# Kernel optimization log

Measured on AMD Instinct MI355X. Metric: run time of the kernel, lower is better.

The kernel has to match this reference:

```python
import jax, jax.numpy as jnp
import numpy as np

N_NODES = 100000


def setup_inputs() -> dict:
    key = jax.random.key(0)
    k1, k2, k3, k4 = jax.random.split(key, 4)
    N, E, D_IN, D_OUT = N_NODES, 3200000, 256, 256
    feature = jax.random.normal(k1, (N, D_IN), dtype=jnp.float32)
    edge_src = jax.random.randint(k2, (E,), 0, N, dtype=jnp.int32)
    edge_dst = jax.random.randint(k3, (E,), 0, N, dtype=jnp.int32)
    W = jax.random.normal(k4, (D_IN, D_OUT), dtype=jnp.float32) * (1.0 / np.sqrt(D_IN))
    b = jnp.zeros((D_OUT,), dtype=jnp.float32)
    return {"feature": feature, "edge_src": edge_src, "edge_dst": edge_dst, "W": W, "b": b}


def reference(feature, edge_src, edge_dst, W, b):
    # update_all(copy_src('h','m'), sum('m','h')): for each node i,
    # h_i = sum over edges (j->i) of feature[j]  -- scatter-add by destination.
    msgs = feature[edge_src]                                   # [E, D_in] (gather)
    agg = jax.ops.segment_sum(msgs, edge_dst, num_segments=N_NODES)  # [N, D_in]
    # apply_nodes: Linear + activation (relu)
    h = jnp.dot(agg, W) + b                                    # [N, D_out]
    return jax.nn.relu(h)
```

## Files before the change

### kernel.cpp

```cpp
#include <hip/hip_runtime.h>

#define D 256
#define GSHIFT 4
#define GSIZE 16
#define TN 16
#define CAPG2 1024
#define CSHIFT 8
#define CBIN 256
#define GPB 16
#define NCMAX 512
#define CAPC 9216
#define NB_P 256

using bf16x8 = __attribute__((ext_vector_type(8))) short;
using f32x4  = __attribute__((ext_vector_type(4))) float;

__device__ inline float bf_lo(unsigned int u) {
    return __builtin_bit_cast(float, u << 16);
}
__device__ inline float bf_hi(unsigned int u) {
    return __builtin_bit_cast(float, u & 0xffff0000u);
}
__device__ inline unsigned short f2bf(float f) {
    unsigned int x = __builtin_bit_cast(unsigned int, f);
    unsigned int r = (x + 0x7fffu + ((x >> 16) & 1u)) >> 16;
    return (unsigned short)r;
}

__global__ __launch_bounds__(256) void part_kernel(
    const int* __restrict__ src, const int* __restrict__ dst,
    int* __restrict__ gcntC, int* __restrict__ csrA,
    const float* __restrict__ feature, unsigned short* __restrict__ fbf, long n8,
    const float* __restrict__ W, unsigned short* __restrict__ Wt,
    int E, int NC, int chunk, int nConvF)
{
    __shared__ int h[NCMAX];
    const int b = blockIdx.x, t = threadIdx.x;

    if (b < NB_P) {
        for (int i = t; i < NC; i += 256) h[i] = 0;
        __syncthreads();
        const int beg = b * chunk;
        const int end = min(beg + chunk, E);
        for (int i = beg + t; i < end; i += 256)
            atomicAdd(&h[dst[i] >> CSHIFT], 1);
        __syncthreads();
        for (int i = t; i < NC; i += 256) {
            int c = h[i];
            h[i] = c ? atomicAdd(&gcntC[i], c) : 0;
        }
        __syncthreads();
        for (int i = beg + t; i < end; i += 256) {
            int d = dst[i];
            int c = d >> CSHIFT;
            int r = atomicAdd(&h[c], 1);
            if (r < CAPC)
                csrA[(size_t)c * CAPC + r] = (src[i] << CSHIFT) | (d & (CBIN - 1));
        }
        return;
    }
    if (b < NB_P + nConvF) {
        long i = (long)(b - NB_P) * 256 + t;
        if (i < n8) {
            const float4* p = reinterpret_cast<const float4*>(feature + i * 8);
            float4 v0 = p[0], v1 = p[1];
            uint4 r;
            r.x = (unsigned int)f2bf(v0.x) | ((unsigned int)f2bf(v0.y) << 16);
            r.y = (unsigned int)f2bf(v0.z) | ((unsigned int)f2bf(v0.w) << 16);
            r.z = (unsigned int)f2bf(v1.x) | ((unsigned int)f2bf(v1.y) << 16);
            r.w = (unsigned int)f2bf(v1.z) | ((unsigned int)f2bf(v1.w) << 16);
            *reinterpret_cast<uint4*>(fbf + i * 8) = r;
        }
        return;
    }
    int i = (b - NB_P - nConvF) * 256 + t;
    if (i < D * D / 4) {
        int n  = i >> 6;
        int k0 = (i & 63) * 4;
        float a  = W[(size_t)(k0 + 0) * D + n];
        float bb = W[(size_t)(k0 + 1) * D + n];
        float c  = W[(size_t)(k0 + 2) * D + n];
        float d  = W[(size_t)(k0 + 3) * D + n];
        uint2 r;
        r.x = (unsigned int)f2bf(a) | ((unsigned int)f2bf(bb) << 16);
        r.y = (unsigned int)f2bf(c) | ((unsigned int)f2bf(d) << 16);
        *reinterpret_cast<uint2*>(Wt + (size_t)n * D + k0) = r;
    }
}

__global__ __launch_bounds__(256) void regroup_kernel(
    const int* __restrict__ csrA, const int* __restrict__ gcntC,
    int* __restrict__ csrB, int* __restrict__ gcnt, int K)
{
    __shared__ int sorted[CAPC];
    __shared__ int h2[GPB], b2[GPB], cur2[GPB];
    const int c = blockIdx.x, t = threadIdx.x;
    const size_t rbeg = (size_t)c * CAPC;
    const int cnt = min(gcntC[c], CAPC);

    if (t < GPB) h2[t] = 0;
    __syncthreads();
    for (int i = t; i < cnt; i += 256)
        atomicAdd(&h2[(csrA[rbeg + i] >> GSHIFT) & (GPB - 1)], 1);
    __syncthreads();
    if (t == 0) {
        int run = 0;
        for (int j = 0; j < GPB; ++j) { b2[j] = run; run += h2[j]; }
    }
    __syncthreads();
    if (t < GPB) cur2[t] = b2[t];
    __syncthreads();
    for (int i = t; i < cnt; i += 256) {
        int p = csrA[rbeg + i];
        int r = atomicAdd(&cur2[(p >> GSHIFT) & (GPB - 1)], 1);
        sorted[r] = p;
    }
    __syncthreads();
    for (int i = t; i < cnt; i += 256) {
        int p = sorted[i];
        int g = (p >> GSHIFT) & (GPB - 1);
        int k = (c << 4) + g;
        int off = i - b2[g];
        if (k < K && off < CAPG2)
            csrB[(size_t)k * CAPG2 + off] = ((p >> CSHIFT) << GSHIFT) | (p & (GSIZE - 1));
    }
    if (t < GPB) {
        int k = (c << 4) + t;
        if (k < K) gcnt[k] = min(h2[t], CAPG2);
    }
}

__global__ __launch_bounds__(256) void agg_gemm_kernel(
    const unsigned short* __restrict__ fbf,
    const int* __restrict__ csrB,
    const int* __restrict__ gcnt,
    const unsigned short* __restrict__ Wt,
    const float* __restrict__ bias,
    float* __restrict__ out, int N)
{
    __shared__ int lsrc[CAPG2];
    __shared__ int nBeg[TN], nCnt[TN], nCur[TN];
    __shared__ unsigned short A[TN][D + 8];

    const int blk  = blockIdx.x;
    const int t    = threadIdx.x;
    const int wave = t >> 6;
    const int lane = t & 63;
    const int sub  = lane & 31;
    const int half = lane >> 5;
    const int node0 = blk * TN;
    const size_t colOff = (size_t)(sub << 3);

    const size_t beg = (size_t)blk * CAPG2;
    const int cnt = min(gcnt[blk], CAPG2);

    if (t < TN) nCnt[t] = 0;
    __syncthreads();
    for (int i = t; i < cnt; i += 256)
        atomicAdd(&nCnt[csrB[beg + i] & (GSIZE - 1)], 1);
    __syncthreads();
    if (t == 0) {
        int run = 0;
        for (int j = 0; j < TN; ++j) { nBeg[j] = run; run += nCnt[j]; }
    }
    __syncthreads();
    if (t < TN) nCur[t] = nBeg[t];
    __syncthreads();
    for (int i = t; i < cnt; i += 256) {
        int p = csrB[beg + i];
        int r = atomicAdd(&nCur[p & (GSIZE - 1)], 1);
        lsrc[r] = p >> GSHIFT;
    }
    __syncthreads();

    for (int ni = 0; ni < 4; ++ni) {
        const int l = (wave << 2) + ni;
        const int node = node0 + l;
        float a0 = 0.f, a1 = 0.f, a2 = 0.f, a3 = 0.f;
        float a4 = 0.f, a5 = 0.f, a6 = 0.f, a7 = 0.f;
        if (node < N) {
            const int b0 = nBeg[l];
            const int c0 = nCnt[l];
            int j = 0;
            for (; j + 3 < c0; j += 4) {
                int s0 = lsrc[b0 + j + half];
                int s1 = lsrc[b0 + j + 2 + half];
                uint4 v0 = *reinterpret_cast<const uint4*>(fbf + ((size_t)s0 << 8) + colOff);
                uint4 v1 = *reinterpret_cast<const uint4*>(fbf + ((size_t)s1 << 8) + colOff);
                a0 += bf_lo(v0.x); a1 += bf_hi(v0.x); a2 += bf_lo(v0.y); a3 += bf_hi(v0.y);
                a4 += bf_lo(v0.z); a5 += bf_hi(v0.z); a6 += bf_lo(v0.w); a7 += bf_hi(v0.w);
                a0 += bf_lo(v1.x); a1 += bf_hi(v1.x); a2 += bf_lo(v1.y); a3 += bf_hi(v1.y);
                a4 += bf_lo(v1.z); a5 += bf_hi(v1.z); a6 += bf_lo(v1.w); a7 += bf_hi(v1.w);
            }
            if (j + 1 < c0) {
                int s0 = lsrc[b0 + j + half];
                uint4 v0 = *reinterpret_cast<const uint4*>(fbf + ((size_t)s0 << 8) + colOff);
                a0 += bf_lo(v0.x); a1 += bf_hi(v0.x); a2 += bf_lo(v0.y); a3 += bf_hi(v0.y);
                a4 += bf_lo(v0.z); a5 += bf_hi(v0.z); a6 += bf_lo(v0.w); a7 += bf_hi(v0.w);
                j += 2;
            }
            if (j < c0 && half == 0) {
                int s0 = lsrc[b0 + j];
                uint4 v0 = *reinterpret_cast<const uint4*>(fbf + ((size_t)s0 << 8) + colOff);
                a0 += bf_lo(v0.x); a1 += bf_hi(v0.x); a2 += bf_lo(v0.y); a3 += bf_hi(v0.y);
                a4 += bf_lo(v0.z); a5 += bf_hi(v0.z); a6 += bf_lo(v0.w); a7 += bf_hi(v0.w);
            }
        }
        a0 += __shfl_xor(a0, 32); a1 += __shfl_xor(a1, 32);
        a2 += __shfl_xor(a2, 32); a3 += __shfl_xor(a3, 32);
        a4 += __shfl_xor(a4, 32); a5 += __shfl_xor(a5, 32);
        a6 += __shfl_xor(a6, 32); a7 += __shfl_xor(a7, 32);
        if (half == 0) {
            uint4 r;
            r.x = (unsigned int)f2bf(a0) | ((unsigned int)f2bf(a1) << 16);
            r.y = (unsigned int)f2bf(a2) | ((unsigned int)f2bf(a3) << 16);
            r.z = (unsigned int)f2bf(a4) | ((unsigned int)f2bf(a5) << 16);
            r.w = (unsigned int)f2bf(a6) | ((unsigned int)f2bf(a7) << 16);
            *reinterpret_cast<uint4*>(&A[l][sub << 3]) = r;
        }
    }
    __syncthreads();

    const int lr = lane & 15;
    const int lg = lane >> 4;

    bf16x8 afr[8];
#pragma unroll
    for (int ks = 0; ks < 8; ++ks)
        afr[ks] = *reinterpret_cast<const bf16x8*>(&A[lr][ks * 32 + lg * 8]);

#pragma unroll
    for (int c = 0; c < 4; ++c) {
        const int ct = (wave << 2) + c;
        f32x4 acc = {0.f, 0.f, 0.f, 0.f};
        const unsigned short* bp = Wt + (size_t)(ct * 16 + lr) * D + lg * 8;
#pragma unroll
        for (int ks = 0; ks < 8; ++ks) {
            bf16x8 bfr = *reinterpret_cast<const bf16x8*>(bp + ks * 32);
            acc = __builtin_amdgcn_mfma_f32_16x16x32_bf16(afr[ks], bfr, acc, 0, 0, 0);
        }
        const float bv = bias[ct * 16 + lr];
#pragma unroll
        for (int jj = 0; jj < 4; ++jj) {
            int row = node0 + lg * 4 + jj;
            if (row < N) {
                float v = acc[jj] + bv;
                out[(size_t)row * D + ct * 16 + lr] = v > 0.f ? v : 0.f;
            }
        }
    }
}

__global__ __launch_bounds__(256) void scatter_kernel(
    const float* __restrict__ feature, const int* __restrict__ src,
    const int* __restrict__ dst, float* __restrict__ agg, int E)
{
    int edge = blockIdx.x * (blockDim.x >> 6) + (threadIdx.x >> 6);
    int lane = threadIdx.x & 63;
    if (edge >= E) return;
    int s = src[edge];
    int d = dst[edge];
    const float4 v = *reinterpret_cast<const float4*>(feature + (size_t)s * D + lane * 4);
    float* o = agg + (size_t)d * D + lane * 4;
    atomicAdd(o + 0, v.x);
    atomicAdd(o + 1, v.y);
    atomicAdd(o + 2, v.z);
    atomicAdd(o + 3, v.w);
}

#define BM 32
__global__ __launch_bounds__(256) void linear_relu_kernel(
    float* __restrict__ h, const float* __restrict__ W,
    const float* __restrict__ b, int n_nodes)
{
    __shared__ float sA[BM][D];
    const int node0 = blockIdx.x * BM;
    const int t = threadIdx.x;
    for (int m = 0; m < BM; ++m) {
        int nd = node0 + m;
        sA[m][t] = (nd < n_nodes) ? h[(size_t)nd * D + t] : 0.0f;
    }
    __syncthreads();
    float acc[BM];
#pragma unroll
    for (int m = 0; m < BM; ++m) acc[m] = 0.0f;
    for (int kk = 0; kk < D; ++kk) {
        float w = W[kk * D + t];
#pragma unroll
        for (int m = 0; m < BM; ++m) acc[m] += sA[m][kk] * w;
    }
    const float bias = b[t];
    for (int m = 0; m < BM; ++m) {
        int nd = node0 + m;
        if (nd < n_nodes) {
            float v = acc[m] + bias;
            h[(size_t)nd * D + t] = v > 0.0f ? v : 0.0f;
        }
    }
}

extern "C" void kernel_launch(void* const* d_in, const int* in_sizes, int n_in,
                              void* d_out, int out_size, void* d_ws, size_t ws_size,
                              hipStream_t stream)
{
    const float* feature = (const float*)d_in[0];
    const int*   src     = (const int*)d_in[1];
    const int*   dst     = (const int*)d_in[2];
    const float* W       = (const float*)d_in[3];
    const float* b       = (const float*)d_in[4];
    float*       out     = (float*)d_out;

    const int E = in_sizes[1];
    const int N = in_sizes[0] / D;
    const int K  = (N + GSIZE - 1) >> GSHIFT;
    const int NC = (N + CBIN - 1) >> CSHIFT;
    const int chunk = (E + NB_P - 1) / NB_P;

    size_t off = 0;
    auto alloc = [&](size_t bytes, size_t align) {
        off = (off + align - 1) / align * align;
        size_t r = off; off += bytes; return r;
    };
    size_t o_gcntC = alloc((size_t)NC * 4, 16);
    size_t o_csrA  = alloc((size_t)NC * CAPC * 4, 16);
    size_t o_gcnt  = alloc((size_t)K * 4, 16);
    size_t o_csrB  = alloc((size_t)K * CAPG2 * 4, 16);
    size_t o_wt    = alloc((size_t)D * D * 2, 16);
    size_t o_fbf   = alloc((size_t)N * D * 2, 16);
    size_t need_full = off;

    char* ws = (char*)d_ws;

    const double mg = (double)E / K;
    const double mc = (double)E / NC;
    const bool cap_ok =
        (mg + 8.0 * __builtin_sqrt(mg) + 16.0 <= (double)CAPG2) &&
        (mc + 8.0 * __builtin_sqrt(mc) + 16.0 <= (double)CAPC) &&
        (NC <= NCMAX);

    if (ws_size >= need_full && cap_ok) {
        int* gcntC = (int*)(ws + o_gcntC);
        int* csrA  = (int*)(ws + o_csrA);
        int* gcnt  = (int*)(ws + o_gcnt);
        int* csrB  = (int*)(ws + o_csrB);
        unsigned short* Wt  = (unsigned short*)(ws + o_wt);
        unsigned short* fbf = (unsigned short*)(ws + o_fbf);

        const long n8 = (long)N * D / 8;
        const int nConvF = (int)((n8 + 255) / 256);
        const int nConvW = (D * D / 4 + 255) / 256;

        hipMemsetAsync(gcntC, 0, (size_t)NC * 4, stream);

        part_kernel<<<NB_P + nConvF + nConvW, 256, 0, stream>>>(
            src, dst, gcntC, csrA, feature, fbf, n8, W, Wt,
            E, NC, chunk, nConvF);

        regroup_kernel<<<NC, 256, 0, stream>>>(csrA, gcntC, csrB, gcnt, K);

        agg_gemm_kernel<<<(N + TN - 1) / TN, 256, 0, stream>>>(
            fbf, csrB, gcnt, Wt, b, out, N);
    } else {
        hipMemsetAsync(d_out, 0, (size_t)out_size * sizeof(float), stream);
        scatter_kernel<<<(E + 3) / 4, 256, 0, stream>>>(feature, src, dst, out, E);
        linear_relu_kernel<<<(N + BM - 1) / BM, 256, 0, stream>>>(out, W, b, N);
    }
}
```

Baseline: 392.0 us.

## Build full per-node CSR in regroup with source-tile sorted edges

The regroup kernel now does a full counting sort within each 256-node bin, keyed by destination node and then by a 4096-node source tile. It writes per-node begin and count arrays plus a CSR of source indices. The aggregation kernel no longer rebuilds a local histogram and sort; it reads node ranges directly and fetches source indices from global memory. Ordering by source tile should improve cache locality of the feature gathers and removes the per-block sort, at the cost of a larger shared histogram in regroup, which lowers its occupancy, and index reads that now go to global memory instead of LDS.

```diff
diff --git a/kernel.cpp b/kernel.cpp
--- a/kernel.cpp
+++ b/kernel.cpp
@@ -1,16 +1,15 @@
 #include <hip/hip_runtime.h>
 
 #define D 256
-#define GSHIFT 4
 #define GSIZE 16
 #define TN 16
-#define CAPG2 1024
 #define CSHIFT 8
 #define CBIN 256
-#define GPB 16
 #define NCMAX 512
 #define CAPC 9216
 #define NB_P 256
+#define TILESHIFT 12
+#define NKEY 8192
 
 using bf16x8 = __attribute__((ext_vector_type(8))) short;
 using f32x4  = __attribute__((ext_vector_type(4))) float;
@@ -90,56 +89,75 @@
 
 __global__ __launch_bounds__(256) void regroup_kernel(
     const int* __restrict__ csrA, const int* __restrict__ gcntC,
-    int* __restrict__ csrB, int* __restrict__ gcnt, int K)
-{
+    int* __restrict__ csrB, int* __restrict__ nodeBeg, int* __restrict__ nodeCnt,
+    int N)
+{
+    __shared__ int h[NKEY];
     __shared__ int sorted[CAPC];
-    __shared__ int h2[GPB], b2[GPB], cur2[GPB];
+    __shared__ int psum[256];
+    __shared__ int nBegL[CBIN], nCntL[CBIN];
     const int c = blockIdx.x, t = threadIdx.x;
     const size_t rbeg = (size_t)c * CAPC;
     const int cnt = min(gcntC[c], CAPC);
 
-    if (t < GPB) h2[t] = 0;
-    __syncthreads();
-    for (int i = t; i < cnt; i += 256)
-        atomicAdd(&h2[(csrA[rbeg + i] >> GSHIFT) & (GPB - 1)], 1);
-    __syncthreads();
-    if (t == 0) {
-        int run = 0;
-        for (int j = 0; j < GPB; ++j) { b2[j] = run; run += h2[j]; }
-    }
-    __syncthreads();
-    if (t < GPB) cur2[t] = b2[t];
+    for (int i = t; i < NKEY; i += 256) h[i] = 0;
     __syncthreads();
     for (int i = t; i < cnt; i += 256) {
         int p = csrA[rbeg + i];
-        int r = atomicAdd(&cur2[(p >> GSHIFT) & (GPB - 1)], 1);
-        sorted[r] = p;
+        int key = ((p & (CBIN - 1)) << 5) | ((p >> CSHIFT) >> TILESHIFT);
+        atomicAdd(&h[key], 1);
+    }
+    __syncthreads();
+    int local = 0;
+#pragma unroll
+    for (int j = 0; j < 32; ++j) local += h[(t << 5) + j];
+    psum[t] = local;
+    nCntL[t] = local;
+    __syncthreads();
+    for (int off = 1; off < 256; off <<= 1) {
+        int v = (t >= off) ? psum[t - off] : 0;
+        __syncthreads();
+        if (t >= off) psum[t] += v;
+        __syncthreads();
+    }
+    int run = (t == 0) ? 0 : psum[t - 1];
+    nBegL[t] = run;
+#pragma unroll
+    for (int j = 0; j < 32; ++j) {
+        int idx = (t << 5) + j;
+        int cc = h[idx];
+        h[idx] = run;
+        run += cc;
     }
     __syncthreads();
     for (int i = t; i < cnt; i += 256) {
-        int p = sorted[i];
-        int g = (p >> GSHIFT) & (GPB - 1);
-        int k = (c << 4) + g;
-        int off = i - b2[g];
-        if (k < K && off < CAPG2)
-            csrB[(size_t)k * CAPG2 + off] = ((p >> CSHIFT) << GSHIFT) | (p & (GSIZE - 1));
-    }
-    if (t < GPB) {
-        int k = (c << 4) + t;
-        if (k < K) gcnt[k] = min(h2[t], CAPG2);
+        int p = csrA[rbeg + i];
+        int key = ((p & (CBIN - 1)) << 5) | ((p >> CSHIFT) >> TILESHIFT);
+        int r = atomicAdd(&h[key], 1);
+        sorted[r] = p >> CSHIFT;
+    }
+    __syncthreads();
+    for (int i = t; i < cnt; i += 256)
+        csrB[rbeg + i] = sorted[i];
+    {
+        int node = (c << CSHIFT) + t;
+        if (node < N) {
+            nodeBeg[node] = (int)(rbeg + nBegL[t]);
+            nodeCnt[node] = nCntL[t];
+        }
     }
 }
 
 __global__ __launch_bounds__(256) void agg_gemm_kernel(
     const unsigned short* __restrict__ fbf,
     const int* __restrict__ csrB,
-    const int* __restrict__ gcnt,
+    const int* __restrict__ nodeBeg,
+    const int* __restrict__ nodeCnt,
     const unsigned short* __restrict__ Wt,
     const float* __restrict__ bias,
     float* __restrict__ out, int N)
 {
-    __shared__ int lsrc[CAPG2];
-    __shared__ int nBeg[TN], nCnt[TN], nCur[TN];
+    __shared__ int nBeg[TN], nCnt[TN];
     __shared__ unsigned short A[TN][D + 8];
 
     const int blk  = blockIdx.x;
@@ -151,25 +169,10 @@
     const int node0 = blk * TN;
     const size_t colOff = (size_t)(sub << 3);
 
-    const size_t beg = (size_t)blk * CAPG2;
-    const int cnt = min(gcnt[blk], CAPG2);
-
-    if (t < TN) nCnt[t] = 0;
-    __syncthreads();
-    for (int i = t; i < cnt; i += 256)
-        atomicAdd(&nCnt[csrB[beg + i] & (GSIZE - 1)], 1);
-    __syncthreads();
-    if (t == 0) {
-        int run = 0;
-        for (int j = 0; j < TN; ++j) { nBeg[j] = run; run += nCnt[j]; }
-    }
-    __syncthreads();
-    if (t < TN) nCur[t] = nBeg[t];
-    __syncthreads();
-    for (int i = t; i < cnt; i += 256) {
-        int p = csrB[beg + i];
-        int r = atomicAdd(&nCur[p & (GSIZE - 1)], 1);
-        lsrc[r] = p >> GSHIFT;
+    if (t < TN) {
+        int node = node0 + t;
+        nBeg[t] = (node < N) ? nodeBeg[node] : 0;
+        nCnt[t] = (node < N) ? nodeCnt[node] : 0;
     }
     __syncthreads();
 
@@ -183,8 +186,8 @@
             const int c0 = nCnt[l];
             int j = 0;
             for (; j + 3 < c0; j += 4) {
-                int s0 = lsrc[b0 + j + half];
-                int s1 = lsrc[b0 + j + 2 + half];
+                int s0 = csrB[b0 + j + half];
+                int s1 = csrB[b0 + j + 2 + half];
                 uint4 v0 = *reinterpret_cast<const uint4*>(fbf + ((size_t)s0 << 8) + colOff);
                 uint4 v1 = *reinterpret_cast<const uint4*>(fbf + ((size_t)s1 << 8) + colOff);
                 a0 += bf_lo(v0.x); a1 += bf_hi(v0.x); a2 += bf_lo(v0.y); a3 += bf_hi(v0.y);
@@ -193,14 +196,14 @@
                 a4 += bf_lo(v1.z); a5 += bf_hi(v1.z); a6 += bf_lo(v1.w); a7 += bf_hi(v1.w);
             }
             if (j + 1 < c0) {
-                int s0 = lsrc[b0 + j + half];
+                int s0 = csrB[b0 + j + half];
                 uint4 v0 = *reinterpret_cast<const uint4*>(fbf + ((size_t)s0 << 8) + colOff);
                 a0 += bf_lo(v0.x); a1 += bf_hi(v0.x); a2 += bf_lo(v0.y); a3 += bf_hi(v0.y);
                 a4 += bf_lo(v0.z); a5 += bf_hi(v0.z); a6 += bf_lo(v0.w); a7 += bf_hi(v0.w);
                 j += 2;
             }
             if (j < c0 && half == 0) {
-                int s0 = lsrc[b0 + j];
+                int s0 = csrB[b0 + j];
                 uint4 v0 = *reinterpret_cast<const uint4*>(fbf + ((size_t)s0 << 8) + colOff);
                 a0 += bf_lo(v0.x); a1 += bf_hi(v0.x); a2 += bf_lo(v0.y); a3 += bf_hi(v0.y);
                 a4 += bf_lo(v0.z); a5 += bf_hi(v0.z); a6 += bf_lo(v0.w); a7 += bf_hi(v0.w);
@@ -312,7 +315,6 @@
 
     const int E = in_sizes[1];
     const int N = in_sizes[0] / D;
-    const int K  = (N + GSIZE - 1) >> GSHIFT;
     const int NC = (N + CBIN - 1) >> CSHIFT;
     const int chunk = (E + NB_P - 1) / NB_P;
 
@@ -323,26 +325,27 @@
     };
     size_t o_gcntC = alloc((size_t)NC * 4, 16);
     size_t o_csrA  = alloc((size_t)NC * CAPC * 4, 16);
-    size_t o_gcnt  = alloc((size_t)K * 4, 16);
-    size_t o_csrB  = alloc((size_t)K * CAPG2 * 4, 16);
+    size_t o_csrB  = alloc((size_t)NC * CAPC * 4, 16);
+    size_t o_nbeg  = alloc((size_t)N * 4, 16);
+    size_t o_ncnt  = alloc((size_t)N * 4, 16);
     size_t o_wt    = alloc((size_t)D * D * 2, 16);
     size_t o_fbf   = alloc((size_t)N * D * 2, 16);
     size_t need_full = off;
 
     char* ws = (char*)d_ws;
 
-    const double mg = (double)E / K;
     const double mc = (double)E / NC;
     const bool cap_ok =
-        (mg + 8.0 * __builtin_sqrt(mg) + 16.0 <= (double)CAPG2) &&
         (mc + 8.0 * __builtin_sqrt(mc) + 16.0 <= (double)CAPC) &&
-        (NC <= NCMAX);
+        (NC <= NCMAX) &&
+        (N <= (32 << TILESHIFT));
 
     if (ws_size >= need_full && cap_ok) {
-        int* gcntC = (int*)(ws + o_gcntC);
-        int* csrA  = (int*)(ws + o_csrA);
-        int* gcnt  = (int*)(ws + o_gcnt);
-        int* csrB  = (int*)(ws + o_csrB);
+        int* gcntC   = (int*)(ws + o_gcntC);
+        int* csrA    = (int*)(ws + o_csrA);
+        int* csrB    = (int*)(ws + o_csrB);
+        int* nodeBeg = (int*)(ws + o_nbeg);
+        int* nodeCnt = (int*)(ws + o_ncnt);
         unsigned short* Wt  = (unsigned short*)(ws + o_wt);
         unsigned short* fbf = (unsigned short*)(ws + o_fbf);
 
@@ -356,10 +359,11 @@
             src, dst, gcntC, csrA, feature, fbf, n8, W, Wt,
             E, NC, chunk, nConvF);
 
-        regroup_kernel<<<NC, 256, 0, stream>>>(csrA, gcntC, csrB, gcnt, K);
+        regroup_kernel<<<NC, 256, 0, stream>>>(
+            csrA, gcntC, csrB, nodeBeg, nodeCnt, N);
 
         agg_gemm_kernel<<<(N + TN - 1) / TN, 256, 0, stream>>>(
-            fbf, csrB, gcnt, Wt, b, out, N);
+            fbf, csrB, nodeBeg, nodeCnt, Wt, b, out, N);
     } else {
         hipMemsetAsync(d_out, 0, (size_t)out_size * sizeof(float), stream);
         scatter_kernel<<<(E + 3) / 4, 256, 0, stream>>>(feature, src, dst, out, E);
```

After: 425.2 us. 1.08x slower.
